# Kernel tuning notes

Measured on AMD Instinct MI355X. Metric: run time of the kernel, lower is better.

The kernel has to match this reference:

```python
import jax, jax.numpy as jnp
import numpy as np
import math

H = 2048; NH = 16; HD = 128; E = 8; K = 2; F = 8192; CAP_F = 1.25
B = 2; S = 2048

def _layernorm(x, scale, bias, eps=1e-5):
    m = jnp.mean(x, axis=-1, keepdims=True)
    v = jnp.var(x, axis=-1, keepdims=True)
    return (x - m) * jax.lax.rsqrt(v + eps) * scale + bias

def _rope(x):
    # x: [B, S, NH, HD]; half-split RoPE, theta=10000
    hd = x.shape[-1]
    pos = jnp.arange(x.shape[1], dtype=jnp.float32)
    freqs = 1.0 / (10000.0 ** (jnp.arange(0, hd // 2, dtype=jnp.float32) / (hd // 2)))
    ang = pos[:, None] * freqs[None, :]              # [S, HD/2]
    cos = jnp.cos(ang)[None, :, None, :]
    sin = jnp.sin(ang)[None, :, None, :]
    x1, x2 = jnp.split(x, 2, axis=-1)
    return jnp.concatenate([x1 * cos - x2 * sin, x1 * sin + x2 * cos], axis=-1)

def setup_inputs() -> dict:
    key = jax.random.key(0)
    ks = jax.random.split(key, 16)
    std = 0.02
    inp = {
        'hidden_states': jax.random.normal(ks[0], (B, S, H), jnp.float32),
        'attention_mask': jnp.ones((B, S), jnp.int32),
        'ln1_scale': jnp.ones((H,), jnp.float32), 'ln1_bias': jnp.zeros((H,), jnp.float32),
        'ln2_scale': jnp.ones((H,), jnp.float32), 'ln2_bias': jnp.zeros((H,), jnp.float32),
        'Wq': jax.random.normal(ks[1], (H, NH * HD), jnp.float32) * std,
        'Wk': jax.random.normal(ks[2], (H, NH * HD), jnp.float32) * std,
        'Wv': jax.random.normal(ks[3], (H, NH * HD), jnp.float32) * std,
        'Wo': jax.random.normal(ks[4], (NH * HD, H), jnp.float32) * std,
        'Wg': jax.random.normal(ks[5], (H, H), jnp.float32) * std,
        'bg': jnp.zeros((H,), jnp.float32),
        'ls_attn': jnp.full((H,), 0.1, jnp.float32),
        'ls_moe': jnp.full((H,), 0.1, jnp.float32),
        'router_w': jax.random.normal(ks[6], (H, E), jnp.float32) * std,
        'W1': jax.random.normal(ks[7], (E, H, F), jnp.float32) * std,
        'b1': jnp.zeros((E, F), jnp.float32),
        'W2': jax.random.normal(ks[8], (E, F, H), jnp.float32) * std,
        'b2': jnp.zeros((E, H), jnp.float32),
    }
    return inp

def _forward(hidden_states, attention_mask, ln1_scale, ln1_bias, ln2_scale, ln2_bias,
             Wq, Wk, Wv, Wo, Wg, bg, ls_attn, ls_moe, router_w, W1, b1, W2, b2):
    b, s, h = hidden_states.shape
    # ---- pre-norm MLA attention + residual ----
    xn = _layernorm(hidden_states, ln1_scale, ln1_bias)
    q = (xn @ Wq).reshape(b, s, NH, HD)
    k = (xn @ Wk).reshape(b, s, NH, HD)
    v = (xn @ Wv).reshape(b, s, NH, HD)
    q = _rope(q); k = _rope(k)
    scores = jnp.einsum('bqhd,bkhd->bhqk', q, k) / math.sqrt(HD)
    causal = jnp.tril(jnp.ones((s, s), bool))
    mask = causal[None, None, :, :] & (attention_mask[:, None, None, :] > 0)
    scores = jnp.where(mask, scores, -1e9)
    attn = jax.nn.softmax(scores, axis=-1)
    ctx = jnp.einsum('bhqk,bkhd->bqhd', attn, v).reshape(b, s, NH * HD)
    attn_out = ctx @ Wo
    attn_out = attn_out * jax.nn.sigmoid(xn @ Wg + bg)   # output gating
    attn_out = attn_out * ls_attn                         # layer scale
    hidden_states = hidden_states + attn_out
    # ---- pre-norm MoE FFN + residual ----
    xn2 = _layernorm(hidden_states, ln2_scale, ln2_bias)
    T = b * s
    x = xn2.reshape(T, h)
    logits = (x @ router_w).astype(jnp.float32)           # [T, E]
    probs = jax.nn.softmax(logits, axis=-1)
    gates, idx = jax.lax.top_k(probs, K)                  # [T, K]
    gates = gates / jnp.sum(gates, axis=-1, keepdims=True)
    cap = int(math.ceil(T * K / E * CAP_F))               # expert capacity
    e_flat = idx.reshape(T * K)
    g_flat = gates.reshape(T * K)
    oh = jax.nn.one_hot(e_flat, E, dtype=jnp.int32)       # [TK, E]
    pos = jnp.sum(jnp.cumsum(oh, axis=0) * oh, axis=-1) - 1
    keep = (pos < cap).astype(x.dtype)
    pos_c = jnp.clip(pos, 0, cap - 1)
    x_rep = jnp.repeat(x, K, axis=0)                      # [TK, H]
    buf = jnp.zeros((E, cap, h), x.dtype).at[e_flat, pos_c].add(x_rep * keep[:, None])
    hmid = jax.nn.gelu(jnp.einsum('ech,ehf->ecf', buf, W1) + b1[:, None, :])
    obuf = jnp.einsum('ecf,efh->ech', hmid, W2) + b2[:, None, :]
    tok = obuf[e_flat, pos_c] * (keep * g_flat)[:, None]  # [TK, H]
    moe_out = tok.reshape(T, K, h).sum(axis=1).reshape(b, s, h)
    moe_out = moe_out * ls_moe
    return hidden_states + moe_out

def reference(hidden_states, attention_mask, ln1_scale, ln1_bias, ln2_scale, ln2_bias,
              Wq, Wk, Wv, Wo, Wg, bg, ls_attn, ls_moe, router_w, W1, b1, W2, b2):
    return _forward(hidden_states, attention_mask, ln1_scale, ln1_bias, ln2_scale, ln2_bias,
                    Wq, Wk, Wv, Wo, Wg, bg, ls_attn, ls_moe, router_w, W1, b1, W2, b2)
```

## Files before the change

### kernel.cpp

```cpp
#include <hip/hip_runtime.h>
#include <hip/hip_fp16.h>

typedef _Float16 f16;
typedef _Float16 half4 __attribute__((ext_vector_type(4)));
typedef _Float16 half8 __attribute__((ext_vector_type(8)));
typedef float floatx4 __attribute__((ext_vector_type(4)));

constexpr int kH  = 2048;
constexpr int kS  = 2048;
constexpr int kB  = 2;
constexpr int kT  = kB * kS;
constexpr int kNH = 16;
constexpr int kHD = 128;
constexpr int kE  = 8;
constexpr int kF  = 8192;
constexpr int kCAP = 1280;
constexpr int kTK = kT * 2;

__device__ __forceinline__ void gload16(const void* g, void* lds_) {
  __builtin_amdgcn_global_load_lds((const __attribute__((address_space(1))) void*)g,
                                   (__attribute__((address_space(3))) void*)lds_,
                                   16, 0, 0);
}

__device__ __forceinline__ void xcd_remap(int& bx, int& by, int& bz) {
  const int gx = gridDim.x, gy = gridDim.y;
  const int nwg = gx * gy * gridDim.z;
  int L = (bz * gy + by) * gx + bx;
  L = (L & 7) * (nwg >> 3) + (L >> 3);
  bz = L / (gx * gy);
  const int r = L - bz * gx * gy;
  by = r / gx;  bx = r - by * gx;
}

__global__ __launch_bounds__(256) void transpose_cvt(
    const float* __restrict__ src, f16* __restrict__ dst,
    int ldS, int ldD, long sZ, long dZ)
{
  __shared__ float tile[64][65];
  src += (long)blockIdx.z * sZ;
  dst += (long)blockIdx.z * dZ;
  const int kb = blockIdx.y * 64, nb = blockIdx.x * 64;
  const int tx = threadIdx.x & 15, ty = threadIdx.x >> 4;
#pragma unroll
  for (int i = 0; i < 4; i++) {
    const int r = ty + i * 16;
    const float4 v = *(const float4*)&src[(long)(kb + r) * ldS + nb + tx * 4];
    tile[r][tx * 4 + 0] = v.x; tile[r][tx * 4 + 1] = v.y;
    tile[r][tx * 4 + 2] = v.z; tile[r][tx * 4 + 3] = v.w;
  }
  __syncthreads();
  const int tx8 = threadIdx.x & 7, ty32 = threadIdx.x >> 3;
#pragma unroll
  for (int i = 0; i < 2; i++) {
    const int n = ty32 + i * 32;
    union { f16 h[8]; float4 v; } pk;
#pragma unroll
    for (int j = 0; j < 8; j++) pk.h[j] = (f16)tile[tx8 * 8 + j][n];
    *(float4*)&dst[(long)(nb + n) * ldD + kb + tx8 * 8] = pk.v;
  }
}

__global__ __launch_bounds__(256) void transpose_f16(
    const f16* __restrict__ src, f16* __restrict__ dst,
    int ldS, int ldD, long sZ, long dZ)
{
  __shared__ f16 tile[64][80];
  src += (long)blockIdx.z * sZ;
  dst += (long)blockIdx.z * dZ;
  const int kb = blockIdx.y * 64, nb = blockIdx.x * 64;
  const int tx = threadIdx.x & 7, ty = threadIdx.x >> 3;
#pragma unroll
  for (int i = 0; i < 2; i++) {
    const int r = ty + i * 32;
    *(half8*)&tile[r][tx * 8] =
        *(const half8*)&src[(long)(kb + r) * ldS + nb + tx * 8];
  }
  __syncthreads();
#pragma unroll
  for (int i = 0; i < 2; i++) {
    const int n = ty + i * 32;
    union { f16 h[8]; float4 v; } pk;
#pragma unroll
    for (int j = 0; j < 8; j++) pk.h[j] = tile[tx * 8 + j][n];
    *(float4*)&dst[(long)(nb + n) * ldD + kb + tx * 8] = pk.v;
  }
}

__global__ __launch_bounds__(256) void ln_kernel(
    const float* __restrict__ x, const float* __restrict__ sc,
    const float* __restrict__ bi, f16* __restrict__ o16, float* __restrict__ o32)
{
  const long row = blockIdx.x;
  const float* xr = x + row * kH;
  const int t = threadIdx.x;
  const float4 u = ((const float4*)xr)[t * 2];
  const float4 v = ((const float4*)xr)[t * 2 + 1];
  float s = u.x + u.y + u.z + u.w + v.x + v.y + v.z + v.w;
  float q = u.x*u.x + u.y*u.y + u.z*u.z + u.w*u.w + v.x*v.x + v.y*v.y + v.z*v.z + v.w*v.w;
#pragma unroll
  for (int m = 1; m < 64; m <<= 1) { s += __shfl_xor(s, m); q += __shfl_xor(q, m); }
  __shared__ float red_s[4], red_q[4];
  const int w = t >> 6, l = t & 63;
  if (l == 0) { red_s[w] = s; red_q[w] = q; }
  __syncthreads();
  s = red_s[0] + red_s[1] + red_s[2] + red_s[3];
  q = red_q[0] + red_q[1] + red_q[2] + red_q[3];
  const float mean = s * (1.f / kH);
  const float var = q * (1.f / kH) - mean * mean;
  const float rstd = rsqrtf(var + 1e-5f);
  const int c = t * 8;
  const float vals[8] = {u.x, u.y, u.z, u.w, v.x, v.y, v.z, v.w};
#pragma unroll
  for (int j = 0; j < 8; j++) {
    const float y = (vals[j] - mean) * rstd * sc[c + j] + bi[c + j];
    o16[row * kH + c + j] = (f16)y;
    if (o32 != nullptr) o32[row * kH + c + j] = y;
  }
}

#define STG(SRC, TILE, KC, PAR, MAT) { \
  const f16* s_ = (SRC) + (long)(TILE) * 64 + (KC) * 32; \
  char* d_ = lds + ((PAR) * 65536 + (MAT) * 32768 + (KC) * 16384) + ldsW; \
  gload16(s_, d_); \
  gload16(s_ + 128 * ldGl, d_ + 8192); }

#define MROW(MH, MM, AF) \
  acc[(MH)*4+(MM)][0] = __builtin_amdgcn_mfma_f32_16x16x32_f16(AF, bf0, acc[(MH)*4+(MM)][0], 0, 0, 0); \
  acc[(MH)*4+(MM)][1] = __builtin_amdgcn_mfma_f32_16x16x32_f16(AF, bf1, acc[(MH)*4+(MM)][1], 0, 0, 0); \
  acc[(MH)*4+(MM)][2] = __builtin_amdgcn_mfma_f32_16x16x32_f16(AF, bf2, acc[(MH)*4+(MM)][2], 0, 0, 0); \
  acc[(MH)*4+(MM)][3] = __builtin_amdgcn_mfma_f32_16x16x32_f16(AF, bf3, acc[(MH)*4+(MM)][3], 0, 0, 0);

#define PH(PAR, KC, MH, RB, STAGE_STMT, VM_STMT) { \
  const char* au_ = lds + ((PAR) * 65536 + (KC) * 16384); \
  const char* bu_ = lds + ((PAR) * 65536 + 32768 + (KC) * 16384); \
  af0 = *(const half8*)(au_ + afoff + (MH) * 4096 +    0); \
  af1 = *(const half8*)(au_ + afoff + (MH) * 4096 + 1024); \
  af2 = *(const half8*)(au_ + afoff + (MH) * 4096 + 2048); \
  af3 = *(const half8*)(au_ + afoff + (MH) * 4096 + 3072); \
  if (RB) { \
    bf0 = *(const half8*)(bu_ + bfoff +    0); \
    bf1 = *(const half8*)(bu_ + bfoff + 1024); \
    bf2 = *(const half8*)(bu_ + bfoff + 2048); \
    bf3 = *(const half8*)(bu_ + bfoff + 3072); \
  } \
  STAGE_STMT; \
  VM_STMT; \
  __builtin_amdgcn_sched_barrier(0); \
  __builtin_amdgcn_s_barrier(); \
  asm volatile("s_waitcnt lgkmcnt(0)" ::: "memory"); \
  __builtin_amdgcn_sched_barrier(0); \
  __builtin_amdgcn_s_setprio(1); \
  MROW(MH, 0, af0) MROW(MH, 1, af1) MROW(MH, 2, af2) MROW(MH, 3, af3) \
  __builtin_amdgcn_s_setprio(0); }

#define VM10 asm volatile("s_waitcnt vmcnt(10)" ::: "memory")
#define VM8  asm volatile("s_waitcnt vmcnt(8)" ::: "memory")
#define VM4  asm volatile("s_waitcnt vmcnt(4)" ::: "memory")
#define VM0  asm volatile("s_waitcnt vmcnt(0)" ::: "memory")
#define NOP (void)0

template <int EPI, bool SPLITK, bool XCD>
__global__ __launch_bounds__(512, 2) void gemm8p_kernel(
    const f16* __restrict__ A, const f16* __restrict__ B, void* __restrict__ Cv,
    const float* __restrict__ bias, const int* __restrict__ rowCount,
    int M, int N, int K, long ldA, long ldB, long aZ, long bZ, long cZ,
    long cZ2, long biasZ)
{
  int bx = blockIdx.x, by = blockIdx.y, bz = blockIdx.z;
  if (XCD) xcd_remap(bx, by, bz);
  const int z = bz;
  const int ze = SPLITK ? (z >> 1) : z;
  if (rowCount != nullptr && (int)(by * 256) >= rowCount[ze]) return;
  __shared__ __align__(16) char lds[131072];
  const long khoff = SPLITK ? (long)(z & 1) * K : 0;
  A += (long)ze * aZ + khoff;  B += (long)ze * bZ + khoff;
  const int tid = threadIdx.x, w = tid >> 6, l = tid & 63;
  const int g = l >> 4, lr = l & 15;
  const long m0 = (long)by * 256, n0 = (long)bx * 256;
  const int wm = (w >> 2) * 128, wn = (w & 3) * 64;

  floatx4 acc[8][4];
#pragma unroll
  for (int i = 0; i < 8; i++)
#pragma unroll
    for (int j = 0; j < 4; j++) acc[i][j] = floatx4{0.f, 0.f, 0.f, 0.f};

  const int swzS = ((l & 3) * 8) ^ (((l >> 3) & 3) << 3);
  const f16* aSrc;
  const f16* bSrc;
  long ldGl;
  {
    const int srow = w * 16 + (l >> 2);
    aSrc = A + (m0 + srow) * ldA + swzS;
    bSrc = B + (n0 + srow) * ldB + swzS;
  }
  ldGl = ldA;
  const int ldsW = w * 1024;
  const int rsw = (g * 16) ^ (((lr >> 1) & 3) << 4);
  const int afoff = wm * 64 + lr * 64 + rsw;
  const int bfoff = wn * 64 + lr * 64 + rsw;
  half8 af0, af1, af2, af3;
  half8 bf0 = half8{0}, bf1 = half8{0}, bf2 = half8{0}, bf3 = half8{0};

  STG(aSrc, 0, 0, 0, 0);
  STG(bSrc, 0, 0, 0, 1);
  STG(aSrc, 0, 1, 0, 0);
  STG(bSrc, 0, 1, 0, 1);
  STG(bSrc, 1, 0, 1, 1);
  STG(aSrc, 1, 0, 1, 0);
  STG(bSrc, 1, 1, 1, 1);
  VM10;
  __builtin_amdgcn_sched_barrier(0);
  __builtin_amdgcn_s_barrier();

  const int NI = K >> 7;
  for (int i = 0; i < NI - 1; i++) {
    const int t0 = 2 * i, t1 = 2 * i + 1;
    PH(0, 0, 0, 1, STG(aSrc, (t1),     1, 1, 0), VM10)
    PH(0, 0, 1, 0, STG(bSrc, (t0 + 2), 0, 0, 1), VM10)
    PH(0, 1, 0, 1, STG(aSrc, (t0 + 2), 0, 0, 0), VM10)
    PH(0, 1, 1, 0, STG(bSrc, (t0 + 2), 1, 0, 1), VM10)
    PH(1, 0, 0, 1, STG(aSrc, (t0 + 2), 1, 0, 0), VM10)
    PH(1, 0, 1, 0, STG(bSrc, (t1 + 2), 0, 1, 1), VM10)
    PH(1, 1, 0, 1, STG(aSrc, (t1 + 2), 0, 1, 0), VM10)
    PH(1, 1, 1, 0, STG(bSrc, (t1 + 2), 1, 1, 1), VM10)
  }
  {
    const int t1 = 2 * (NI - 1) + 1;
    PH(0, 0, 0, 1, STG(aSrc, (t1), 1, 1, 0), VM8)
    PH(0, 0, 1, 0, NOP, NOP)
    PH(0, 1, 0, 1, NOP, VM4)
    PH(0, 1, 1, 0, NOP, NOP)
    PH(1, 0, 0, 1, NOP, VM0)
    PH(1, 0, 1, 0, NOP, NOP)
    PH(1, 1, 0, 1, NOP, NOP)
    PH(1, 1, 1, 0, NOP, NOP)
  }

  const long crow = m0 + wm + g * 4;
  const long ccol = n0 + wn + lr;
  float* c32 = (float*)Cv + (long)ze * cZ + (SPLITK ? (long)(z & 1) * cZ2 : 0);
  f16* ch = (f16*)Cv + (long)ze * cZ + (SPLITK ? (long)(z & 1) * cZ2 : 0);
#pragma unroll
  for (int mi = 0; mi < 8; mi++)
#pragma unroll
    for (int ni = 0; ni < 4; ni++)
#pragma unroll
      for (int j = 0; j < 4; j++) {
        const long r = crow + mi * 16 + j;
        const long c = ccol + ni * 16;
        float v = acc[mi][ni][j];
        if (EPI == 0) {
          c32[r * N + c] = v;
        } else if (EPI == 2) {
          v += bias[(long)ze * biasZ + c];
          const float u2 = 1.5957691216057308f * (v + 0.044715f * v * v * v);
          const float sg = 1.f / (1.f + __expf(-u2));
          ((f16*)Cv)[(long)ze * cZ + r * N + c] = (f16)(v * sg);
        } else if (EPI == 3) {
          v += bias[(long)ze * biasZ + c];
          ((f16*)Cv)[(long)ze * cZ + r * N + c] = (f16)v;
        } else {
          ch[r * N + c] = (f16)v;
        }
      }
}
#undef STG
#undef MROW
#undef PH
#undef VM10
#undef VM8
#undef VM4
#undef VM0
#undef NOP

__global__ void rope_table_kernel(float* __restrict__ ct, float* __restrict__ st) {
  const int i = blockIdx.x * 256 + threadIdx.x;
  if (i >= kS * 64) return;
  const int s = i >> 6, f = i & 63;
  const double freq = exp(-0.14391156831212787 * (double)f);
  const double ang = (double)s * freq;
  ct[i] = (float)cos(ang);
  st[i] = (float)sin(ang);
}

__global__ __launch_bounds__(256) void rope_kernel(
    const f16* __restrict__ q, const f16* __restrict__ k,
    const float* __restrict__ ct, const float* __restrict__ st,
    f16* __restrict__ qr, f16* __restrict__ kr)
{
  const long t = blockIdx.x;
  const int s = (int)(t & (kS - 1)), b = (int)(t >> 11);
  for (int u = threadIdx.x; u < kNH * 64; u += 256) {
    const int h = u >> 6, i = u & 63;
    const float c = ct[s * 64 + i], sn = st[s * 64 + i];
    const long src = t * kH + h * kHD + i;
    const long dst = (((long)(b * kNH + h)) * kS + s) * kHD + i;
    float x1 = (float)q[src], x2 = (float)q[src + 64];
    qr[dst]      = (f16)((x1 * c - x2 * sn) * 0.08838834764831845f);
    qr[dst + 64] = (f16)((x1 * sn + x2 * c) * 0.08838834764831845f);
    x1 = (float)k[src]; x2 = (float)k[src + 64];
    kr[dst]      = (f16)(x1 * c - x2 * sn);
    kr[dst + 64] = (f16)(x1 * sn + x2 * c);
  }
}

__global__ __launch_bounds__(256) void attn_kernel(
    const f16* __restrict__ q_r, const f16* __restrict__ k_r,
    const f16* __restrict__ v_t, f16* __restrict__ ctx)
{
  __shared__ f16 Ks[64 * 128];
  __shared__ f16 Vs[128 * 64];
  __shared__ f16 Ps[4][1024];
  int qt = blockIdx.x, h = blockIdx.y, b = blockIdx.z;
  xcd_remap(qt, h, b);
  const int bh = b * kNH + h;
  const int tid = threadIdx.x, w = tid >> 6, l = tid & 63;
  const int g = l >> 4, lr = l & 15;
  const long q0 = (long)qt * 64;
  const f16* qbase = q_r + ((long)bh * kS + q0 + w * 16 + lr) * kHD;
  half8 qf[4];
#pragma unroll
  for (int kc = 0; kc < 4; kc++) qf[kc] = *(const half8*)(qbase + kc * 32 + g * 8);
  floatx4 acc[8];
#pragma unroll
  for (int i = 0; i < 8; i++) acc[i] = floatx4{0.f, 0.f, 0.f, 0.f};
  float mrun[4], lrun[4];
#pragma unroll
  for (int j = 0; j < 4; j++) { mrun[j] = -1e30f; lrun[j] = 0.f; }
  f16* pw = Ps[w];

  for (int kt = 0; kt <= qt; kt++) {
    const long k0 = (long)kt * 64;
#pragma unroll
    for (int c = 0; c < 4; c++) {
      const int cc = w * 4 + c;
      const int row = cc * 4 + (l >> 4);
      const int wb = (l & 15) * 16;
      const int src = (wb ^ ((row & 7) << 4)) >> 1;
      gload16(k_r + ((long)bh * kS + k0 + row) * kHD + src, Ks + cc * 512);
    }
#pragma unroll
    for (int c = 0; c < 4; c++) {
      const int cc = w * 4 + c;
      const int row = cc * 8 + (l >> 3);
      const int wb = (l & 7) * 16;
      const int src = (wb ^ ((row & 7) << 4)) >> 1;
      gload16(v_t + ((long)bh * kHD + row) * kS + k0 + src, Vs + cc * 512);
    }
    asm volatile("s_waitcnt vmcnt(0)" ::: "memory");
    __syncthreads();

    floatx4 sfr[4];
#pragma unroll
    for (int f = 0; f < 4; f++) {
      floatx4 s4 = floatx4{0.f, 0.f, 0.f, 0.f};
      const int row = f * 16 + lr;
#pragma unroll
      for (int kc = 0; kc < 4; kc++) {
        const half8 kfq = *(const half8*)((const char*)Ks + row * 256 +
                            ((kc * 64 + g * 16) ^ ((row & 7) << 4)));
        s4 = __builtin_amdgcn_mfma_f32_16x16x32_f16(qf[kc], kfq, s4, 0, 0, 0);
      }
      sfr[f] = s4;
    }
    if (kt == qt) {
#pragma unroll
      for (int f = 0; f < 4; f++) {
        const int key = kt * 64 + f * 16 + lr;
#pragma unroll
        for (int j = 0; j < 4; j++) {
          const int qrow = qt * 64 + w * 16 + g * 4 + j;
          if (key > qrow) sfr[f][j] = -1e30f;
        }
      }
    }
    float al[4];
#pragma unroll
    for (int j = 0; j < 4; j++) {
      float pm = fmaxf(fmaxf(sfr[0][j], sfr[1][j]), fmaxf(sfr[2][j], sfr[3][j]));
      pm = fmaxf(pm, __shfl_xor(pm, 1)); pm = fmaxf(pm, __shfl_xor(pm, 2));
      pm = fmaxf(pm, __shfl_xor(pm, 4)); pm = fmaxf(pm, __shfl_xor(pm, 8));
      const float mn = fmaxf(mrun[j], pm);
      al[j] = __expf(mrun[j] - mn);
      mrun[j] = mn;
      float rs = 0.f;
#pragma unroll
      for (int f = 0; f < 4; f++) {
        const float p = __expf(sfr[f][j] - mn);
        sfr[f][j] = p; rs += p;
      }
      rs += __shfl_xor(rs, 1); rs += __shfl_xor(rs, 2);
      rs += __shfl_xor(rs, 4); rs += __shfl_xor(rs, 8);
      lrun[j] = lrun[j] * al[j] + rs;
    }
#pragma unroll
    for (int nf = 0; nf < 8; nf++)
#pragma unroll
      for (int j = 0; j < 4; j++) acc[nf][j] *= al[j];
#pragma unroll
    for (int f = 0; f < 4; f++)
#pragma unroll
      for (int j = 0; j < 4; j++) {
        const int row = g * 4 + j;
        const int byteoff = (row * 128 + (f * 16 + lr) * 2) ^ ((row & 7) << 4);
        *(f16*)((char*)pw + byteoff) = (f16)sfr[f][j];
      }
#pragma unroll
    for (int kc = 0; kc < 2; kc++) {
      const half8 pf = *(const half8*)((const char*)pw + lr * 128 +
                         ((kc * 64 + g * 16) ^ ((lr & 7) << 4)));
#pragma unroll
      for (int nf = 0; nf < 8; nf++) {
        const int vrow = nf * 16 + lr;
        const half8 vfr = *(const half8*)((const char*)Vs + vrow * 128 +
                            ((kc * 64 + g * 16) ^ ((vrow & 7) << 4)));
        acc[nf] = __builtin_amdgcn_mfma_f32_16x16x32_f16(pf, vfr, acc[nf], 0, 0, 0);
      }
    }
    __syncthreads();
  }
  const long orow = (long)b * kS + q0 + w * 16;
#pragma unroll
  for (int j = 0; j < 4; j++) {
    const float inv = 1.0f / lrun[j];
    const int r = g * 4 + j;
#pragma unroll
    for (int nf = 0; nf < 8; nf++)
      ctx[(orow + r) * kH + h * kHD + nf * 16 + lr] = (f16)(acc[nf][j] * inv);
  }
}

__global__ __launch_bounds__(256) void combine1_kernel(
    const float* __restrict__ hid, const f16* __restrict__ a0,
    const f16* __restrict__ a1, const f16* __restrict__ glin,
    const float* __restrict__ bg, const float* __restrict__ ls,
    float* __restrict__ out)
{
  const long i = (long)blockIdx.x * 256 + threadIdx.x;
  const float4 hv = ((const float4*)hid)[i];
  const half4 av = ((const half4*)a0)[i];
  const half4 aw = ((const half4*)a1)[i];
  const half4 gv = ((const half4*)glin)[i];
  const int c = (int)(i & 511);
  const float4 lv = ((const float4*)ls)[c];
  const float4 bv = ((const float4*)bg)[c];
  float4 o;
  o.x = hv.x + lv.x * ((float)av[0] + (float)aw[0]) / (1.f + __expf(-((float)gv[0] + bv.x)));
  o.y = hv.y + lv.y * ((float)av[1] + (float)aw[1]) / (1.f + __expf(-((float)gv[1] + bv.y)));
  o.z = hv.z + lv.z * ((float)av[2] + (float)aw[2]) / (1.f + __expf(-((float)gv[2] + bv.z)));
  o.w = hv.w + lv.w * ((float)av[3] + (float)aw[3]) / (1.f + __expf(-((float)gv[3] + bv.w)));
  ((float4*)out)[i] = o;
}

__global__ __launch_bounds__(256) void router_kernel(
    const float* __restrict__ x, const float* __restrict__ rw,
    int* __restrict__ eidx, float* __restrict__ gates)
{
  const int t = blockIdx.x * 4 + (threadIdx.x >> 6);
  const int l = threadIdx.x & 63;
  const float* xr = x + (long)t * kH;
  float a[8] = {0.f, 0.f, 0.f, 0.f, 0.f, 0.f, 0.f, 0.f};
  for (int it = 0; it < kH / 64; it++) {
    const float xv = xr[it * 64 + l];
    const float* r = rw + (long)(it * 64 + l) * kE;
#pragma unroll
    for (int e = 0; e < 8; e++) a[e] += xv * r[e];
  }
#pragma unroll
  for (int e = 0; e < 8; e++)
#pragma unroll
    for (int m = 1; m < 64; m <<= 1) a[e] += __shfl_xor(a[e], m);
  if (l == 0) {
    float mx = a[0];
#pragma unroll
    for (int e = 1; e < 8; e++) mx = fmaxf(mx, a[e]);
    float p[8];
#pragma unroll
    for (int e = 0; e < 8; e++) p[e] = __expf(a[e] - mx);
    int i1 = 0; float v1 = p[0];
#pragma unroll
    for (int e = 1; e < 8; e++) if (p[e] > v1) { v1 = p[e]; i1 = e; }
    int i2 = -1; float v2 = -1.f;
#pragma unroll
    for (int e = 0; e < 8; e++) if (e != i1 && p[e] > v2) { v2 = p[e]; i2 = e; }
    const float inv = 1.f / (v1 + v2);
    eidx[t * 2] = i1; eidx[t * 2 + 1] = i2;
    gates[t * 2] = v1 * inv; gates[t * 2 + 1] = v2 * inv;
  }
}

__global__ void scan_kernel(const int* __restrict__ eidx, int* __restrict__ slot,
                            int* __restrict__ counts)
{
  const int l = threadIdx.x;
  int base[8] = {0, 0, 0, 0, 0, 0, 0, 0};
  const unsigned long long lt = (1ull << l) - 1ull;
  for (int it = 0; it < kTK / 64; it++) {
    const int i = it * 64 + l;
    const int e = eidx[i];
    int mypos = 0;
#pragma unroll
    for (int ex = 0; ex < 8; ex++) {
      const unsigned long long mk = __ballot(e == ex);
      if (e == ex) mypos = base[ex] + __popcll(mk & lt);
      base[ex] += __popcll(mk);
    }
    slot[i] = (mypos < kCAP) ? e * kCAP + mypos : -1;
  }
  if (l == 0) {
#pragma unroll
    for (int ex = 0; ex < 8; ex++) counts[ex] = min(base[ex], kCAP);
  }
}

__global__ __launch_bounds__(256) void scatter_kernel(
    const f16* __restrict__ xh, const int* __restrict__ slot, f16* __restrict__ buf)
{
  const int i = blockIdx.x;
  const int s = slot[i];
  if (s < 0) return;
  const long t = i >> 1;
  ((half8*)(buf + (long)s * kH))[threadIdx.x] =
      ((const half8*)(xh + t * kH))[threadIdx.x];
}

__global__ __launch_bounds__(256) void combine2_kernel(
    const float* __restrict__ hid2, const f16* __restrict__ P0,
    const f16* __restrict__ P1, const int* __restrict__ slot,
    const float* __restrict__ gates, const float* __restrict__ b2,
    const float* __restrict__ ls, float* __restrict__ out)
{
  const int t = blockIdx.x;
  const int c = threadIdx.x * 8;
  float m[8] = {0.f, 0.f, 0.f, 0.f, 0.f, 0.f, 0.f, 0.f};
#pragma unroll
  for (int ks = 0; ks < 2; ks++) {
    const int s = slot[t * 2 + ks];
    if (s < 0) continue;
    const float gte = gates[t * 2 + ks];
    const int e = s / kCAP;
    const long ro = (long)s * kH + c;
    const half8 p0 = *(const half8*)&P0[ro];
    const half8 p1 = *(const half8*)&P1[ro];
    const float4 ba = *(const float4*)&b2[e * kH + c];
    const float4 bb = *(const float4*)&b2[e * kH + c + 4];
    m[0] += gte * ((float)p0[0] + (float)p1[0] + ba.x);
    m[1] += gte * ((float)p0[1] + (float)p1[1] + ba.y);
    m[2] += gte * ((float)p0[2] + (float)p1[2] + ba.z);
    m[3] += gte * ((float)p0[3] + (float)p1[3] + ba.w);
    m[4] += gte * ((float)p0[4] + (float)p1[4] + bb.x);
    m[5] += gte * ((float)p0[5] + (float)p1[5] + bb.y);
    m[6] += gte * ((float)p0[6] + (float)p1[6] + bb.z);
    m[7] += gte * ((float)p0[7] + (float)p1[7] + bb.w);
  }
  const float* hp = hid2 + (long)t * kH + c;
  float* op = out + (long)t * kH + c;
#pragma unroll
  for (int j = 0; j < 8; j++) op[j] = hp[j] + ls[c + j] * m[j];
}

extern "C" void kernel_launch(void* const* d_in, const int* in_sizes, int n_in,
                              void* d_out, int out_size, void* d_ws, size_t ws_size,
                              hipStream_t stream)
{
  (void)in_sizes; (void)n_in;
  const float* hidden   = (const float*)d_in[0];
  const float* ln1s     = (const float*)d_in[2];
  const float* ln1b     = (const float*)d_in[3];
  const float* ln2s     = (const float*)d_in[4];
  const float* ln2b     = (const float*)d_in[5];
  const float* Wq       = (const float*)d_in[6];
  const float* Wk       = (const float*)d_in[7];
  const float* Wv       = (const float*)d_in[8];
  const float* Wo       = (const float*)d_in[9];
  const float* Wg       = (const float*)d_in[10];
  const float* bg       = (const float*)d_in[11];
  const float* ls_attn  = (const float*)d_in[12];
  const float* ls_moe   = (const float*)d_in[13];
  const float* router_w = (const float*)d_in[14];
  const float* W1       = (const float*)d_in[15];
  const float* b1       = (const float*)d_in[16];
  const float* W2       = (const float*)d_in[17];
  const float* b2       = (const float*)d_in[18];

  char* ws = (char*)d_ws;
  size_t off = 0;
  auto take = [&](size_t b) { size_t r = off; off += (b + 255) & ~(size_t)255; return r; };
  const size_t o_wT   = take(5ULL * kH * kH * 2);
  const size_t o_w1t  = take((size_t)kE * kF * kH * 2);
  const size_t o_w2t  = take((size_t)kE * kH * kF * 2);
  const size_t o_xn   = take((size_t)kT * kH * 2);
  const size_t o_qkvg = take(4ULL * kT * kH * 4);
  const size_t o_tab  = take(2ULL * kS * 64 * 4);
  const size_t o_qr   = take(3ULL * kT * kH * 2);
  const size_t o_ctx  = take((size_t)kT * kH * 2);
  const size_t o_h2   = take((size_t)kT * kH * 4);
  const size_t o_sm   = take(1 << 20);
  const size_t o_hmid = take((size_t)kE * kCAP * kF * 2);
  if (off > ws_size) { hipMemsetAsync(d_out, 0xFF, (size_t)out_size * 4, stream); return; }

  f16* wT    = (f16*)(ws + o_wT);
  f16* w1t   = (f16*)(ws + o_w1t);
  f16* w2t   = (f16*)(ws + o_w2t);
  f16* xn    = (f16*)(ws + o_xn);
  float* tabc = (float*)(ws + o_tab);
  float* tabs = tabc + (size_t)kS * 64;
  f16* qr  = (f16*)(ws + o_qr);
  f16* kr  = qr + (size_t)kT * kH;
  f16* vt  = kr + (size_t)kT * kH;
  f16* ctx = (f16*)(ws + o_ctx);
  float* h2 = (float*)(ws + o_h2);
  int* eidx    = (int*)(ws + o_sm);
  float* gates = (float*)(ws + o_sm + 65536);
  int* slot    = (int*)(ws + o_sm + 131072);
  int* counts  = (int*)(ws + o_sm + 196608);
  f16* hmid = (f16*)(ws + o_hmid);

  const size_t S2 = (size_t)kT * kH * 2;
  char* R = ws + o_qkvg;
  f16* qh = (f16*)(R + 0 * S2);
  f16* kh = (f16*)(R + 1 * S2);
  f16* vh = (f16*)(R + 2 * S2);
  f16* gh = (f16*)(R + 3 * S2);
  float* x2f = (float*)(R + 4 * S2);
  f16* x2h   = (f16*)(R + 6 * S2);
  f16* woPh  = (f16*)(R + 0 * S2);
  f16* buf  = qr;
  f16* P0h = (f16*)(ws + o_w1t);
  f16* P1h = P0h + (size_t)kE * kCAP * kH;

  const long HH = (long)kH * kH;

  transpose_cvt<<<dim3(32, 32, 1), 256, 0, stream>>>(Wq, wT + 0 * HH, kH, kH, 0, 0);
  transpose_cvt<<<dim3(32, 32, 1), 256, 0, stream>>>(Wk, wT + 1 * HH, kH, kH, 0, 0);
  transpose_cvt<<<dim3(32, 32, 1), 256, 0, stream>>>(Wv, wT + 2 * HH, kH, kH, 0, 0);
  transpose_cvt<<<dim3(32, 32, 1), 256, 0, stream>>>(Wg, wT + 3 * HH, kH, kH, 0, 0);
  transpose_cvt<<<dim3(32, 32, 1), 256, 0, stream>>>(Wo, wT + 4 * HH, kH, kH, 0, 0);
  transpose_cvt<<<dim3(kF / 64, kH / 64, kE), 256, 0, stream>>>(
      W1, w1t, kF, kH, (long)kH * kF, (long)kF * kH);
  transpose_cvt<<<dim3(kH / 64, kF / 64, kE), 256, 0, stream>>>(
      W2, w2t, kH, kF, (long)kF * kH, (long)kH * kF);
  ln_kernel<<<kT, 256, 0, stream>>>(hidden, ln1s, ln1b, xn, nullptr);
  gemm8p_kernel<4, false, true><<<dim3(kH / 256, kT / 256, 4), 512, 0, stream>>>(
      xn, wT, qh, nullptr, nullptr, kT, kH, kH, kH, kH,
      0L, HH, (long)kT * kH, 0L, 0L);
  rope_table_kernel<<<(kS * 64 + 255) / 256, 256, 0, stream>>>(tabc, tabs);
  rope_kernel<<<kT, 256, 0, stream>>>(qh, kh, tabc, tabs, qr, kr);
  for (int b = 0; b < kB; b++)
    transpose_f16<<<dim3(kHD / 64, kS / 64, kNH), 256, 0, stream>>>(
        vh + (size_t)b * kS * kH, vt + (size_t)b * kNH * kHD * kS,
        kH, kS, 128L, (long)kHD * kS);
  attn_kernel<<<dim3(kS / 64, kNH, kB), 256, 0, stream>>>(qr, kr, vt, ctx);
  gemm8p_kernel<4, true, true><<<dim3(kH / 256, kT / 256, 2), 512, 0, stream>>>(
      ctx, wT + 4 * HH, woPh, nullptr, nullptr, kT, kH, 1024, kH, kH,
      0L, 0L, 0L, (long)kT * kH, 0L);
  combine1_kernel<<<(kT * kH / 4) / 256, 256, 0, stream>>>(
      hidden, woPh, woPh + (size_t)kT * kH, gh, bg, ls_attn, h2);
  ln_kernel<<<kT, 256, 0, stream>>>(h2, ln2s, ln2b, x2h, x2f);
  router_kernel<<<kT / 4, 256, 0, stream>>>(x2f, router_w, eidx, gates);
  scan_kernel<<<1, 64, 0, stream>>>(eidx, slot, counts);
  scatter_kernel<<<kTK, 256, 0, stream>>>(x2h, slot, buf);
  gemm8p_kernel<2, false, false><<<dim3(kF / 256, kCAP / 256, kE), 512, 0, stream>>>(
      buf, w1t, hmid, b1, counts, kCAP, kF, kH, kH, kH,
      (long)kCAP * kH, (long)kF * kH, (long)kCAP * kF, 0L, (long)kF);
  gemm8p_kernel<4, true, false><<<dim3(kH / 256, kCAP / 256, 2 * kE), 512, 0, stream>>>(
      hmid, w2t, P0h, nullptr, counts, kCAP, kH, 4096, kF, kF,
      (long)kCAP * kF, (long)kH * kF, (long)kCAP * kH, (long)kE * kCAP * kH, 0L);
  combine2_kernel<<<kT, 256, 0, stream>>>(
      h2, P0h, P1h, slot, gates, b2, ls_moe, (float*)d_out);
}
```

Baseline: 1.532 ms.

## Split MoE down-projection four ways on K and batch attention weight transposes

Generalizes the GEMM split-K template from 2 to an arbitrary factor and splits the expert W2 GEMM four ways to raise block count (8x5x32 grid instead of 8x5x16). Combine2 now sums four fp16 partials instead of two. The five attention weight transposes are merged into one launch, and the W1/W2 transposes are moved later in the stream next to their consumers. Extra partial-buffer traffic and fp16 rounding of more partials are the cost, and the partial buffer now needs twice the workspace.

```diff
diff --git a/kernel.cpp b/kernel.cpp
--- a/kernel.cpp
+++ b/kernel.cpp
@@ -58,6 +58,42 @@
 #pragma unroll
     for (int j = 0; j < 8; j++) pk.h[j] = (f16)tile[tx8 * 8 + j][n];
     *(float4*)&dst[(long)(nb + n) * ldD + kb + tx8 * 8] = pk.v;
+  }
+}
+
+__global__ __launch_bounds__(256) void transpose_cvt5(
+    const float* __restrict__ s0, const float* __restrict__ s1,
+    const float* __restrict__ s2, const float* __restrict__ s3,
+    const float* __restrict__ s4, f16* __restrict__ dst)
+{
+  __shared__ float tile[64][65];
+  const float* src;
+  switch (blockIdx.z) {
+    case 0: src = s0; break;
+    case 1: src = s1; break;
+    case 2: src = s2; break;
+    case 3: src = s3; break;
+    default: src = s4; break;
+  }
+  dst += (long)blockIdx.z * kH * kH;
+  const int kb = blockIdx.y * 64, nb = blockIdx.x * 64;
+  const int tx = threadIdx.x & 15, ty = threadIdx.x >> 4;
+#pragma unroll
+  for (int i = 0; i < 4; i++) {
+    const int r = ty + i * 16;
+    const float4 v = *(const float4*)&src[(long)(kb + r) * kH + nb + tx * 4];
+    tile[r][tx * 4 + 0] = v.x; tile[r][tx * 4 + 1] = v.y;
+    tile[r][tx * 4 + 2] = v.z; tile[r][tx * 4 + 3] = v.w;
+  }
+  __syncthreads();
+  const int tx8 = threadIdx.x & 7, ty32 = threadIdx.x >> 3;
+#pragma unroll
+  for (int i = 0; i < 2; i++) {
+    const int n = ty32 + i * 32;
+    union { f16 h[8]; float4 v; } pk;
+#pragma unroll
+    for (int j = 0; j < 8; j++) pk.h[j] = (f16)tile[tx8 * 8 + j][n];
+    *(float4*)&dst[(long)(nb + n) * kH + kb + tx8 * 8] = pk.v;
   }
 }
 
@@ -160,7 +196,7 @@
 #define VM0  asm volatile("s_waitcnt vmcnt(0)" ::: "memory")
 #define NOP (void)0
 
-template <int EPI, bool SPLITK, bool XCD>
+template <int EPI, int SK, bool XCD>
 __global__ __launch_bounds__(512, 2) void gemm8p_kernel(
     const f16* __restrict__ A, const f16* __restrict__ B, void* __restrict__ Cv,
     const float* __restrict__ bias, const int* __restrict__ rowCount,
@@ -170,10 +206,11 @@
   int bx = blockIdx.x, by = blockIdx.y, bz = blockIdx.z;
   if (XCD) xcd_remap(bx, by, bz);
   const int z = bz;
-  const int ze = SPLITK ? (z >> 1) : z;
+  const int ze = z / SK;
+  const int kq = z % SK;
   if (rowCount != nullptr && (int)(by * 256) >= rowCount[ze]) return;
   __shared__ __align__(16) char lds[131072];
-  const long khoff = SPLITK ? (long)(z & 1) * K : 0;
+  const long khoff = (long)kq * K;
   A += (long)ze * aZ + khoff;  B += (long)ze * bZ + khoff;
   const int tid = threadIdx.x, w = tid >> 6, l = tid & 63;
   const int g = l >> 4, lr = l & 15;
@@ -240,8 +277,8 @@
 
   const long crow = m0 + wm + g * 4;
   const long ccol = n0 + wn + lr;
-  float* c32 = (float*)Cv + (long)ze * cZ + (SPLITK ? (long)(z & 1) * cZ2 : 0);
-  f16* ch = (f16*)Cv + (long)ze * cZ + (SPLITK ? (long)(z & 1) * cZ2 : 0);
+  float* c32 = (float*)Cv + (long)ze * cZ + (long)kq * cZ2;
+  f16* ch = (f16*)Cv + (long)ze * cZ + (long)kq * cZ2;
 #pragma unroll
   for (int mi = 0; mi < 8; mi++)
 #pragma unroll
@@ -527,10 +564,10 @@
 }
 
 __global__ __launch_bounds__(256) void combine2_kernel(
-    const float* __restrict__ hid2, const f16* __restrict__ P0,
-    const f16* __restrict__ P1, const int* __restrict__ slot,
-    const float* __restrict__ gates, const float* __restrict__ b2,
-    const float* __restrict__ ls, float* __restrict__ out)
+    const float* __restrict__ hid2, const f16* __restrict__ P,
+    const int* __restrict__ slot, const float* __restrict__ gates,
+    const float* __restrict__ b2, const float* __restrict__ ls,
+    float* __restrict__ out, long pS)
 {
   const int t = blockIdx.x;
   const int c = threadIdx.x * 8;
@@ -542,18 +579,19 @@
     const float gte = gates[t * 2 + ks];
     const int e = s / kCAP;
     const long ro = (long)s * kH + c;
-    const half8 p0 = *(const half8*)&P0[ro];
-    const half8 p1 = *(const half8*)&P1[ro];
+    float acc8[8];
     const float4 ba = *(const float4*)&b2[e * kH + c];
     const float4 bb = *(const float4*)&b2[e * kH + c + 4];
-    m[0] += gte * ((float)p0[0] + (float)p1[0] + ba.x);
-    m[1] += gte * ((float)p0[1] + (float)p1[1] + ba.y);
-    m[2] += gte * ((float)p0[2] + (float)p1[2] + ba.z);
-    m[3] += gte * ((float)p0[3] + (float)p1[3] + ba.w);
-    m[4] += gte * ((float)p0[4] + (float)p1[4] + bb.x);
-    m[5] += gte * ((float)p0[5] + (float)p1[5] + bb.y);
-    m[6] += gte * ((float)p0[6] + (float)p1[6] + bb.z);
-    m[7] += gte * ((float)p0[7] + (float)p1[7] + bb.w);
+    acc8[0] = ba.x; acc8[1] = ba.y; acc8[2] = ba.z; acc8[3] = ba.w;
+    acc8[4] = bb.x; acc8[5] = bb.y; acc8[6] = bb.z; acc8[7] = bb.w;
+#pragma unroll
+    for (int q = 0; q < 4; q++) {
+      const half8 p = *(const half8*)&P[q * pS + ro];
+#pragma unroll
+      for (int j = 0; j < 8; j++) acc8[j] += (float)p[j];
+    }
+#pragma unroll
+    for (int j = 0; j < 8; j++) m[j] += gte * acc8[j];
   }
   const float* hp = hid2 + (long)t * kH + c;
   float* op = out + (long)t * kH + c;
@@ -628,22 +666,14 @@
   f16* x2h   = (f16*)(R + 6 * S2);
   f16* woPh  = (f16*)(R + 0 * S2);
   f16* buf  = qr;
-  f16* P0h = (f16*)(ws + o_w1t);
-  f16* P1h = P0h + (size_t)kE * kCAP * kH;
+  f16* Ph = (f16*)(ws + o_w1t);
+  const long pS = (long)kE * kCAP * kH;
 
   const long HH = (long)kH * kH;
 
-  transpose_cvt<<<dim3(32, 32, 1), 256, 0, stream>>>(Wq, wT + 0 * HH, kH, kH, 0, 0);
-  transpose_cvt<<<dim3(32, 32, 1), 256, 0, stream>>>(Wk, wT + 1 * HH, kH, kH, 0, 0);
-  transpose_cvt<<<dim3(32, 32, 1), 256, 0, stream>>>(Wv, wT + 2 * HH, kH, kH, 0, 0);
-  transpose_cvt<<<dim3(32, 32, 1), 256, 0, stream>>>(Wg, wT + 3 * HH, kH, kH, 0, 0);
-  transpose_cvt<<<dim3(32, 32, 1), 256, 0, stream>>>(Wo, wT + 4 * HH, kH, kH, 0, 0);
-  transpose_cvt<<<dim3(kF / 64, kH / 64, kE), 256, 0, stream>>>(
-      W1, w1t, kF, kH, (long)kH * kF, (long)kF * kH);
-  transpose_cvt<<<dim3(kH / 64, kF / 64, kE), 256, 0, stream>>>(
-      W2, w2t, kH, kF, (long)kF * kH, (long)kH * kF);
   ln_kernel<<<kT, 256, 0, stream>>>(hidden, ln1s, ln1b, xn, nullptr);
-  gemm8p_kernel<4, false, true><<<dim3(kH / 256, kT / 256, 4), 512, 0, stream>>>(
+  transpose_cvt5<<<dim3(32, 32, 5), 256, 0, stream>>>(Wq, Wk, Wv, Wg, Wo, wT);
+  gemm8p_kernel<4, 1, true><<<dim3(kH / 256, kT / 256, 4), 512, 0, stream>>>(
       xn, wT, qh, nullptr, nullptr, kT, kH, kH, kH, kH,
       0L, HH, (long)kT * kH, 0L, 0L);
   rope_table_kernel<<<(kS * 64 + 255) / 256, 256, 0, stream>>>(tabc, tabs);
@@ -653,7 +683,7 @@
         vh + (size_t)b * kS * kH, vt + (size_t)b * kNH * kHD * kS,
         kH, kS, 128L, (long)kHD * kS);
   attn_kernel<<<dim3(kS / 64, kNH, kB), 256, 0, stream>>>(qr, kr, vt, ctx);
-  gemm8p_kernel<4, true, true><<<dim3(kH / 256, kT / 256, 2), 512, 0, stream>>>(
+  gemm8p_kernel<4, 2, true><<<dim3(kH / 256, kT / 256, 2), 512, 0, stream>>>(
       ctx, wT + 4 * HH, woPh, nullptr, nullptr, kT, kH, 1024, kH, kH,
       0L, 0L, 0L, (long)kT * kH, 0L);
   combine1_kernel<<<(kT * kH / 4) / 256, 256, 0, stream>>>(
@@ -662,12 +692,16 @@
   router_kernel<<<kT / 4, 256, 0, stream>>>(x2f, router_w, eidx, gates);
   scan_kernel<<<1, 64, 0, stream>>>(eidx, slot, counts);
   scatter_kernel<<<kTK, 256, 0, stream>>>(x2h, slot, buf);
-  gemm8p_kernel<2, false, false><<<dim3(kF / 256, kCAP / 256, kE), 512, 0, stream>>>(
+  transpose_cvt<<<dim3(kF / 64, kH / 64, kE), 256, 0, stream>>>(
+      W1, w1t, kF, kH, (long)kH * kF, (long)kF * kH);
+  gemm8p_kernel<2, 1, false><<<dim3(kF / 256, kCAP / 256, kE), 512, 0, stream>>>(
       buf, w1t, hmid, b1, counts, kCAP, kF, kH, kH, kH,
       (long)kCAP * kH, (long)kF * kH, (long)kCAP * kF, 0L, (long)kF);
-  gemm8p_kernel<4, true, false><<<dim3(kH / 256, kCAP / 256, 2 * kE), 512, 0, stream>>>(
-      hmid, w2t, P0h, nullptr, counts, kCAP, kH, 4096, kF, kF,
-      (long)kCAP * kF, (long)kH * kF, (long)kCAP * kH, (long)kE * kCAP * kH, 0L);
+  transpose_cvt<<<dim3(kH / 64, kF / 64, kE), 256, 0, stream>>>(
+      W2, w2t, kH, kF, (long)kF * kH, (long)kH * kF);
+  gemm8p_kernel<4, 4, false><<<dim3(kH / 256, kCAP / 256, 4 * kE), 512, 0, stream>>>(
+      hmid, w2t, Ph, nullptr, counts, kCAP, kH, 2048, kF, kF,
+      (long)kCAP * kF, (long)kH * kF, (long)kCAP * kH, pS, 0L);
   combine2_kernel<<<kT, 256, 0, stream>>>(
-      h2, P0h, P1h, slot, gates, b2, ls_moe, (float*)d_out);
-}
+      h2, Ph, slot, gates, b2, ls_moe, (float*)d_out, pS);
+}
```

After: 1.520 ms. About the same (-0.8%).
